# Performance work log

Measured on AMD Instinct MI355X. Metric: run time of the kernel, lower is better.

The kernel has to match this reference:

```python
import jax, jax.numpy as jnp
import numpy as np

B, H, T, TE = 48, 256, 512, 256  # batch*nodes, hidden=node_dim, timesteps, time_emb_dim


def timestep_embedding(ts, dim, max_positions=10000):
    half = dim // 2
    freqs = jnp.exp(jnp.arange(half, dtype=jnp.float32) * (-np.log(max_positions) / (half - 1)))
    e = ts.astype(jnp.float32)[:, None] * freqs[None, :]
    return jnp.concatenate([jnp.sin(e), jnp.cos(e)], axis=-1)  # [len, dim]


def mlp2(x, W1, b1, W2, b2):
    # 2-layer MLP: Linear -> SiLU -> Linear
    return jax.nn.silu(x @ W1 + b1) @ W2 + b2


def setup_inputs() -> dict:
    key = jax.random.key(0)
    ks = jax.random.split(key, 16)
    s = lambda k, shp, fan: (jax.random.normal(k, shp, dtype=jnp.float32) / np.sqrt(fan))
    return {
        "x": jax.random.normal(ks[0], (B, 3, T), dtype=jnp.float32),
        "h": jax.random.normal(ks[1], (B, H, T), dtype=jnp.float32),
        "qW1": s(ks[2], (H, H), H), "qb1": jnp.zeros((H,), jnp.float32),
        "qW2": s(ks[3], (H, H), H), "qb2": jnp.zeros((H,), jnp.float32),
        "kW1": s(ks[4], (H, H), H), "kb1": jnp.zeros((H,), jnp.float32),
        "kW2": s(ks[5], (H, H), H), "kb2": jnp.zeros((H,), jnp.float32),
        "vW1": s(ks[6], (H, H), H), "vb1": jnp.zeros((H,), jnp.float32),
        "vW2": s(ks[7], (H, H), H), "vb2": jnp.zeros((H,), jnp.float32),
        "xW1": s(ks[8], (H, H), H), "xb1": jnp.zeros((H,), jnp.float32),
        "xW2": s(ks[9], (H, 1), H), "xb2": jnp.zeros((1,), jnp.float32),
        "teW": s(ks[10], (TE, H), TE), "teb": jnp.zeros((H,), jnp.float32),
    }


def reference(x, h, qW1, qb1, qW2, qb2, kW1, kb1, kW2, kb2,
              vW1, vb1, vW2, vb2, xW1, xb1, xW2, xb2, teW, teb):
    Bb, _, Tt = x.shape
    rel_range = jnp.arange(-Tt + 1, Tt)
    emb_rel = timestep_embedding(rel_range, teW.shape[0]) @ teW + teb  # [2T-1, H]
    idx = jnp.arange(Tt)[:, None] - jnp.arange(Tt)[None, :] + (Tt - 1)  # [T, T]
    rel_pos = emb_rel[idx]  # [T, T, H]

    hm = h.transpose(0, 2, 1).reshape(Bb * Tt, -1)  # merge_time_dim: [BT, H]
    q = mlp2(hm, qW1, qb1, qW2, qb2)
    k = mlp2(hm, kW1, kb1, kW2, kb2)
    v = mlp2(hm, vW1, vb1, vW2, vb2)
    v_x = mlp2(v, xW1, xb1, xW2, xb2)  # [BT, 1]

    qt = q.reshape(Bb, Tt, -1)   # [B, T, H]
    kt = k.reshape(Bb, Tt, -1)
    vt = v.reshape(Bb, Tt, -1)

    base = jnp.einsum('bth,bsh->bts', qt, kt)  # [B, T, T]
    rel_logits = qt @ emb_rel.T  # [B, T, 2T-1]
    bias_logits = jnp.take_along_axis(
        rel_logits, jnp.broadcast_to(idx[None], (Bb, Tt, Tt)), axis=2)
    alpha = jax.nn.softmax(base + bias_logits, axis=-1)  # [B, T, T]

    std_vs = jnp.einsum('bts,bsh->bht', alpha, vt)       # [B, H, T]
    bias_h = jnp.einsum('bts,tsh->bht', alpha, rel_pos)  # [B, H, T]
    h_new = h + std_vs + bias_h

    # equivariant coord update: sum_s alpha[b,t,s]*(x[b,c,t]-x[b,c,s])*v_x[b,s]
    vx = v_x.reshape(Bb, Tt)               # [B, T]
    w = alpha * vx[:, None, :]             # [B, T, T]
    x_update = x * jnp.sum(w, axis=-1)[:, None, :] - jnp.einsum('bts,bcs->bct', w, x)
    x_new = x + x_update
    return (x_new, h_new)
```

## Files before the change

kernel.cpp:

```cpp
#include <hip/hip_runtime.h>
#include <math.h>

#define NB 48
#define HD 256
#define TS 512

typedef _Float16 f16x8 __attribute__((ext_vector_type(8)));
typedef float    f32x4 __attribute__((ext_vector_type(4)));

__device__ inline unsigned short f2h(float f) {
  union { _Float16 h; unsigned short u; } v; v.h = (_Float16)f; return v.u;
}
__device__ inline float h2f(unsigned short u) {
  union { unsigned short u; _Float16 h; } v; v.u = u; return (float)v.h;
}

#define ETS 1056

__device__ __forceinline__ void gll16(const void* g, void* l) {
  __builtin_amdgcn_global_load_lds(
      (const __attribute__((address_space(1))) unsigned int*)g,
      (__attribute__((address_space(3))) unsigned int*)l, 16, 0, 0);
}

__global__ __launch_bounds__(256) void k_prep(
    const float* __restrict__ h, unsigned short* __restrict__ hmH,
    float* __restrict__ vxZ,
    const float* __restrict__ w0, const float* __restrict__ w1,
    const float* __restrict__ w2, const float* __restrict__ w3,
    const float* __restrict__ w4, const float* __restrict__ w5,
    const float* __restrict__ w6, const float* __restrict__ w7,
    unsigned short* __restrict__ WtH, unsigned short* __restrict__ SC)
{
  const int gid = blockIdx.x;
  const int tid = threadIdx.x;

  if (gid < 128) {
    const int cf = tid & 127, half = tid >> 7;
    const float f = expf((float)cf * (-9.210340371976184f / 127.0f));
#pragma unroll
    for (int rr = 0; rr < 8; ++rr) {
      int r = gid * 8 + rr;
      float ang = (float)(r - (TS - 1)) * f;
      float val = (r == 1023) ? 0.0f : (half ? cosf(ang) : sinf(ang));
      SC[r * 256 + tid] = f2h(val);
    }
    return;
  }
  if (gid < 1664) {
    const int idx = gid - 128;
    const int bx = idx & 3, by = (idx >> 2) & 7, bz = idx >> 5;
    __shared__ float t[32 * 132];
    const int t0 = bx * 128, c0 = by * 32, b = bz;
    if (by == 0 && bz == 0) {
      float4* vz = (float4*)(vxZ + ((size_t)bx * 256 + tid) * 24);
#pragma unroll
      for (int i = 0; i < 6; ++i) vz[i] = make_float4(0.f, 0.f, 0.f, 0.f);
    }
#pragma unroll
    for (int i = 0; i < 4; ++i) {
      int cl = i * 8 + (tid >> 5);
      int t4 = (tid & 31) * 4;
      float4 v = *(const float4*)&h[((size_t)b * 256 + c0 + cl) * 512 + t0 + t4];
      t[cl * 132 + t4 + 0] = v.x; t[cl * 132 + t4 + 1] = v.y;
      t[cl * 132 + t4 + 2] = v.z; t[cl * 132 + t4 + 3] = v.w;
    }
    __syncthreads();
#pragma unroll
    for (int i = 0; i < 16; ++i) {
      int tl = i * 8 + (tid >> 5);
      int cl = tid & 31;
      hmH[((size_t)b * 512 + t0 + tl) * 256 + c0 + cl] = f2h(t[cl * 132 + tl]);
    }
    return;
  }
  {
    const int idx = gid - 1664;
    const int kx = idx & 3, ny = (idx >> 2) & 3, mat = idx >> 4;
    const float* W = (mat == 0) ? w0 : (mat == 1) ? w1 : (mat == 2) ? w2 :
                     (mat == 3) ? w3 : (mat == 4) ? w4 : (mat == 5) ? w5 :
                     (mat == 6) ? w6 : w7;
    unsigned short* dst = WtH + (size_t)mat * 65536;
    __shared__ float t[64 * 68];
    const int k0 = kx * 64, n0 = ny * 64;
#pragma unroll
    for (int i = 0; i < 4; ++i) {
      int kr = i * 16 + (tid >> 4);
      int nc = (tid & 15) * 4;
      float4 v = *(const float4*)&W[(size_t)(k0 + kr) * 256 + n0 + nc];
      t[kr * 68 + nc + 0] = v.x; t[kr * 68 + nc + 1] = v.y;
      t[kr * 68 + nc + 2] = v.z; t[kr * 68 + nc + 3] = v.w;
    }
    __syncthreads();
#pragma unroll
    for (int i = 0; i < 4; ++i) {
      int nr = i * 16 + (tid >> 4);
      int kc = (tid & 15) * 4;
#pragma unroll
      for (int j = 0; j < 4; ++j)
        dst[(size_t)(n0 + nr) * 256 + k0 + kc + j] = f2h(t[(kc + j) * 68 + nr]);
    }
  }
}

struct MJob {
  const unsigned short* A; const unsigned short* W1; const float* b1;
  const unsigned short* W2; const float* b2;
  unsigned short* outB; unsigned short* outT;
};
struct MJobs { MJob j[3]; };

__global__ __launch_bounds__(256) void k_mlp2(MJobs jobs)
{
  __shared__ __align__(16) char Wst[32768];
  __shared__ __align__(16) char Ast[8192];
  __shared__ __align__(16) char Hst[64 * 528];

  const MJob jb = jobs.j[blockIdx.y];
  const int tid  = threadIdx.x;
  const int lane = tid & 63;
  const int w    = tid >> 6;
  const int rq   = lane & 15;
  const int kq   = lane >> 4;
  const int m0   = blockIdx.x * 64;
  const char* Ag  = (const char*)jb.A  + (size_t)m0 * 512;
  const char* W1g = (const char*)jb.W1;
  const char* W2g = (const char*)jb.W2;

  f32x4 acc[4][4];
#pragma unroll
  for (int mi = 0; mi < 4; ++mi)
#pragma unroll
    for (int ni = 0; ni < 4; ++ni) acc[mi][ni] = (f32x4){0.f, 0.f, 0.f, 0.f};

  for (int kt = 0; kt < 4; ++kt) {
    __syncthreads();
#pragma unroll
    for (int i = 0; i < 2; ++i) {
      int c = i * 256 + tid;
      int row = c >> 3, ch = c & 7;
      int colg = (ch * 16) ^ ((row & 7) << 4);
      gll16(Ag + (size_t)row * 512 + kt * 128 + colg, Ast + i * 4096 + w * 1024);
    }
#pragma unroll
    for (int i = 0; i < 8; ++i) {
      int c = i * 256 + tid;
      int row = c >> 3, ch = c & 7;
      int colg = (ch * 16) ^ ((row & 7) << 4);
      gll16(W1g + (size_t)row * 512 + kt * 128 + colg, Wst + i * 4096 + w * 1024);
    }
    __syncthreads();
#pragma unroll
    for (int ks = 0; ks < 2; ++ks) {
      const int kb = ks * 64 + kq * 16;
      f16x8 af[4], bfr[4];
#pragma unroll
      for (int mi = 0; mi < 4; ++mi) {
        int row = mi * 16 + rq;
        af[mi] = *(const f16x8*)(Ast + row * 128 + (kb ^ ((row & 7) << 4)));
      }
#pragma unroll
      for (int ni = 0; ni < 4; ++ni) {
        int row = w * 64 + ni * 16 + rq;
        bfr[ni] = *(const f16x8*)(Wst + row * 128 + (kb ^ ((row & 7) << 4)));
      }
#pragma unroll
      for (int mi = 0; mi < 4; ++mi)
#pragma unroll
        for (int ni = 0; ni < 4; ++ni)
          acc[mi][ni] = __builtin_amdgcn_mfma_f32_16x16x32_f16(
              af[mi], bfr[ni], acc[mi][ni], 0, 0, 0);
    }
  }
  {
#pragma unroll
    for (int ni = 0; ni < 4; ++ni) {
      const int n = w * 64 + ni * 16 + rq;
      const float bv = jb.b1[n];
#pragma unroll
      for (int mi = 0; mi < 4; ++mi)
#pragma unroll
        for (int j = 0; j < 4; ++j) {
          float vl = acc[mi][ni][j] + bv;
          vl = vl / (1.0f + __expf(-vl));
          int m = mi * 16 + kq * 4 + j;
          *(unsigned short*)(Hst + m * 528 + n * 2) = f2h(vl);
        }
    }
  }
#pragma unroll
  for (int mi = 0; mi < 4; ++mi)
#pragma unroll
    for (int ni = 0; ni < 4; ++ni) acc[mi][ni] = (f32x4){0.f, 0.f, 0.f, 0.f};

  for (int kt = 0; kt < 4; ++kt) {
    __syncthreads();
#pragma unroll
    for (int i = 0; i < 8; ++i) {
      int c = i * 256 + tid;
      int row = c >> 3, ch = c & 7;
      int colg = (ch * 16) ^ ((row & 7) << 4);
      gll16(W2g + (size_t)row * 512 + kt * 128 + colg, Wst + i * 4096 + w * 1024);
    }
    __syncthreads();
#pragma unroll
    for (int ks = 0; ks < 2; ++ks) {
      const int kb = ks * 64 + kq * 16;
      f16x8 af[4], bfr[4];
#pragma unroll
      for (int mi = 0; mi < 4; ++mi) {
        int row = mi * 16 + rq;
        af[mi] = *(const f16x8*)(Hst + row * 528 + kt * 128 + kb);
      }
#pragma unroll
      for (int ni = 0; ni < 4; ++ni) {
        int row = w * 64 + ni * 16 + rq;
        bfr[ni] = *(const f16x8*)(Wst + row * 128 + (kb ^ ((row & 7) << 4)));
      }
#pragma unroll
      for (int mi = 0; mi < 4; ++mi)
#pragma unroll
        for (int ni = 0; ni < 4; ++ni)
          acc[mi][ni] = __builtin_amdgcn_mfma_f32_16x16x32_f16(
              af[mi], bfr[ni], acc[mi][ni], 0, 0, 0);
    }
  }

  const int bb = m0 >> 9;
  const int tbase = m0 & 511;
#pragma unroll
  for (int ni = 0; ni < 4; ++ni) {
    const int n = w * 64 + ni * 16 + rq;
    const float bv = jb.b2[n];
#pragma unroll
    for (int mi = 0; mi < 4; ++mi) {
      float vl4[4];
#pragma unroll
      for (int j = 0; j < 4; ++j) vl4[j] = acc[mi][ni][j] + bv;
#pragma unroll
      for (int j = 0; j < 4; ++j) {
        int m = m0 + mi * 16 + kq * 4 + j;
        jb.outB[(size_t)m * 256 + n] = f2h(vl4[j]);
      }
      if (jb.outT) {
        ushort4 o;
        o.x = f2h(vl4[0]); o.y = f2h(vl4[1]);
        o.z = f2h(vl4[2]); o.w = f2h(vl4[3]);
        *(ushort4*)&jb.outT[((size_t)(bb * 256 + n) << 9) +
                            tbase + mi * 16 + kq * 4] = o;
      }
    }
  }
}

struct GJob {
  const unsigned short* A; const unsigned short* Wt; const float* bias;
  unsigned short* outB; unsigned short* outE;
  const float* vxW; float* vxOut;
  int act; int mMax;
};
struct GJobs { GJob j[2]; };

__global__ __launch_bounds__(512) void k_gemm(GJobs jobs)
{
  __shared__ __align__(16) char AsB[16384];
  __shared__ __align__(16) char WsB[32768];

  const GJob jb = jobs.j[blockIdx.z];
  const int m0 = blockIdx.x * 128;
  if (m0 >= jb.mMax) return;

  const int tid  = threadIdx.x;
  const int lane = tid & 63;
  const int w    = tid >> 6;
  const int wr   = w >> 2, wc = w & 3;
  const int rq   = lane & 15;
  const int kq   = lane >> 4;

  const char* Ag = (const char*)jb.A + (size_t)m0 * 512;
  const char* Wg = (const char*)jb.Wt;

  f32x4 acc[4][4];
#pragma unroll
  for (int mi = 0; mi < 4; ++mi)
#pragma unroll
    for (int ni = 0; ni < 4; ++ni) acc[mi][ni] = (f32x4){0.f, 0.f, 0.f, 0.f};

  for (int kt = 0; kt < 4; ++kt) {
    __syncthreads();
#pragma unroll
    for (int i = 0; i < 2; ++i) {
      int c = i * 512 + tid;
      int row = c >> 3, ch = c & 7;
      int colg = (ch * 16) ^ ((row & 7) << 4);
      gll16(Ag + (size_t)row * 512 + kt * 128 + colg, AsB + i * 8192 + w * 1024);
    }
#pragma unroll
    for (int i = 0; i < 4; ++i) {
      int c = i * 512 + tid;
      int row = c >> 3, ch = c & 7;
      int colg = (ch * 16) ^ ((row & 7) << 4);
      gll16(Wg + (size_t)row * 512 + kt * 128 + colg, WsB + i * 8192 + w * 1024);
    }
    __syncthreads();
#pragma unroll
    for (int ks = 0; ks < 2; ++ks) {
      const int kb = ks * 64 + kq * 16;
      f16x8 af[4], bfr[4];
#pragma unroll
      for (int mi = 0; mi < 4; ++mi) {
        int row = wr * 64 + mi * 16 + rq;
        af[mi] = *(const f16x8*)(AsB + row * 128 + (kb ^ ((row & 7) << 4)));
      }
#pragma unroll
      for (int ni = 0; ni < 4; ++ni) {
        int row = wc * 64 + ni * 16 + rq;
        bfr[ni] = *(const f16x8*)(WsB + row * 128 + (kb ^ ((row & 7) << 4)));
      }
#pragma unroll
      for (int mi = 0; mi < 4; ++mi)
#pragma unroll
        for (int ni = 0; ni < 4; ++ni)
          acc[mi][ni] = __builtin_amdgcn_mfma_f32_16x16x32_f16(
              af[mi], bfr[ni], acc[mi][ni], 0, 0, 0);
    }
  }

  float bv[4];
#pragma unroll
  for (int ni = 0; ni < 4; ++ni)
    bv[ni] = jb.bias[wc * 64 + ni * 16 + rq];

  float vxp_[4][4];
#pragma unroll
  for (int mi = 0; mi < 4; ++mi)
#pragma unroll
    for (int j = 0; j < 4; ++j) vxp_[mi][j] = 0.f;

#pragma unroll
  for (int mi = 0; mi < 4; ++mi) {
#pragma unroll
    for (int ni = 0; ni < 4; ++ni) {
      const int n = wc * 64 + ni * 16 + rq;
      float vl4[4];
#pragma unroll
      for (int j = 0; j < 4; ++j) {
        float vl = acc[mi][ni][j] + bv[ni];
        if (jb.act) vl = vl / (1.0f + __expf(-vl));
        vl4[j] = vl;
      }
      const int mb = m0 + wr * 64 + mi * 16 + kq * 4;
      if (jb.outB) {
#pragma unroll
        for (int j = 0; j < 4; ++j)
          jb.outB[(size_t)(mb + j) * 256 + n] = f2h(vl4[j]);
      }
      if (jb.outE) {
#pragma unroll
        for (int j = 0; j < 4; ++j)
          jb.outE[(size_t)n * ETS + mb + j] = f2h(vl4[j]);
      }
      if (jb.vxOut) {
        float wq = jb.vxW[n];
#pragma unroll
        for (int j = 0; j < 4; ++j) vxp_[mi][j] = fmaf(vl4[j], wq, vxp_[mi][j]);
      }
    }
  }

  if (jb.vxOut) {
#pragma unroll
    for (int mi = 0; mi < 4; ++mi)
#pragma unroll
      for (int j = 0; j < 4; ++j) {
        float s = vxp_[mi][j];
        s += __shfl_xor(s, 1); s += __shfl_xor(s, 2);
        s += __shfl_xor(s, 4); s += __shfl_xor(s, 8);
        if (rq == 0)
          atomicAdd(&jb.vxOut[m0 + wr * 64 + mi * 16 + kq * 4 + j], s);
      }
  }
}

__global__ __launch_bounds__(256, 2) void k_attn6(
    const float* __restrict__ xin, const float* __restrict__ hin,
    const unsigned short* __restrict__ qH, const unsigned short* __restrict__ kH,
    const unsigned short* __restrict__ vtH, const float* __restrict__ vxm,
    const float* __restrict__ xb2p,
    const unsigned short* __restrict__ embB, const unsigned short* __restrict__ embT,
    float* __restrict__ xout, float* __restrict__ hout)
{
  __shared__ __align__(16) char smem[70656];
  float* S  = (float*)smem;
  unsigned short* Pb = (unsigned short*)smem;
  unsigned short* Pe = (unsigned short*)(smem + 33280);

  const int tid  = threadIdx.x;
  const int lane = tid & 63;
  const int w    = tid >> 6;
  const int rq   = lane & 15;
  const int kq   = lane >> 4;
  const int id = blockIdx.x;
  const int t0 = ((id >> 3) & 15) * 32;
  const int b  = (id & 7) + 8 * (id >> 7);
  const int sw = w * 128;

  f16x8 q0[8], q1[8];
  {
    const size_t qo = ((size_t)(b * TS + t0 + rq) << 8) + kq * 8;
#pragma unroll
    for (int ks = 0; ks < 8; ++ks) {
      q0[ks] = *(const f16x8*)(qH + qo + ks * 32);
      q1[ks] = *(const f16x8*)(qH + qo + 4096 + ks * 32);
    }
  }

  f32x4 a0[8], a1[8];
#pragma unroll
  for (int ni = 0; ni < 8; ++ni) {
    a0[ni] = (f32x4){0.f, 0.f, 0.f, 0.f};
    a1[ni] = (f32x4){0.f, 0.f, 0.f, 0.f};
  }
  {
    const unsigned short* kp = kH + ((size_t)(b * TS + sw + rq) << 8) + kq * 8;
    f16x8 kA[8], kB[8];
#pragma unroll
    for (int ni = 0; ni < 8; ++ni) kA[ni] = *(const f16x8*)(kp + ni * 4096);
#pragma unroll
    for (int ni = 0; ni < 8; ++ni) kB[ni] = *(const f16x8*)(kp + ni * 4096 + 32);
#pragma unroll
    for (int ks = 0; ks < 8; ks += 2) {
#pragma unroll
      for (int ni = 0; ni < 8; ++ni) {
        a0[ni] = __builtin_amdgcn_mfma_f32_16x16x32_f16(q0[ks], kA[ni], a0[ni], 0, 0, 0);
        a1[ni] = __builtin_amdgcn_mfma_f32_16x16x32_f16(q1[ks], kA[ni], a1[ni], 0, 0, 0);
        if (ks + 2 < 8) kA[ni] = *(const f16x8*)(kp + ni * 4096 + (ks + 2) * 32);
      }
#pragma unroll
      for (int ni = 0; ni < 8; ++ni) {
        a0[ni] = __builtin_amdgcn_mfma_f32_16x16x32_f16(q0[ks + 1], kB[ni], a0[ni], 0, 0, 0);
        a1[ni] = __builtin_amdgcn_mfma_f32_16x16x32_f16(q1[ks + 1], kB[ni], a1[ni], 0, 0, 0);
        if (ks + 3 < 8) kB[ni] = *(const f16x8*)(kp + ni * 4096 + (ks + 3) * 32);
      }
    }
  }

  const int rbR = t0 - sw + 384;
  const unsigned short* ep = embB + ((size_t)(rbR + rq) << 8) + kq * 8;
  f16x8 eA[10], eB[10];
#pragma unroll
  for (int f = 0; f < 10; ++f) eA[f] = *(const f16x8*)(ep + f * 4096);
#pragma unroll
  for (int ni = 0; ni < 8; ++ni)
#pragma unroll
    for (int j = 0; j < 4; ++j) {
      S[(kq * 4 + j) * 524 + sw + ni * 16 + rq]        = a0[ni][j];
      S[(16 + kq * 4 + j) * 524 + sw + ni * 16 + rq]   = a1[ni][j];
    }
#pragma unroll
  for (int f = 0; f < 10; ++f) eB[f] = *(const f16x8*)(ep + f * 4096 + 32);

  f32x4 r0[9], r1[9];
#pragma unroll
  for (int ni = 0; ni < 9; ++ni) {
    r0[ni] = (f32x4){0.f, 0.f, 0.f, 0.f};
    r1[ni] = (f32x4){0.f, 0.f, 0.f, 0.f};
  }
#pragma unroll
  for (int ks = 0; ks < 8; ks += 2) {
#pragma unroll
    for (int f = 0; f < 10; ++f) {
      if (f < 9) r0[f] = __builtin_amdgcn_mfma_f32_16x16x32_f16(q0[ks], eA[f], r0[f], 0, 0, 0);
      if (f > 0) r1[f - 1] = __builtin_amdgcn_mfma_f32_16x16x32_f16(q1[ks], eA[f], r1[f - 1], 0, 0, 0);
      if (ks + 2 < 8) eA[f] = *(const f16x8*)(ep + f * 4096 + (ks + 2) * 32);
    }
#pragma unroll
    for (int f = 0; f < 10; ++f) {
      if (f < 9) r0[f] = __builtin_amdgcn_mfma_f32_16x16x32_f16(q0[ks + 1], eB[f], r0[f], 0, 0, 0);
      if (f > 0) r1[f - 1] = __builtin_amdgcn_mfma_f32_16x16x32_f16(q1[ks + 1], eB[f], r1[f - 1], 0, 0, 0);
      if (ks + 3 < 8) eB[f] = *(const f16x8*)(ep + f * 4096 + (ks + 3) * 32);
    }
  }

  asm volatile("s_waitcnt lgkmcnt(0)" ::: "memory");
  __builtin_amdgcn_sched_barrier(0);
#pragma unroll
  for (int ni = 0; ni < 9; ++ni)
#pragma unroll
    for (int j = 0; j < 4; ++j) {
      int tp  = kq * 4 + j;
      int slw = tp + 127 - (ni * 16 + rq);
      if (slw >= 0 && slw < 128) {
        S[tp * 524 + sw + slw]        += r0[ni][j];
        S[(16 + tp) * 524 + sw + slw] += r1[ni][j];
      }
    }
  __syncthreads();

  const int row16 = tid >> 4, tx = tid & 15;
  float p0[32], p1[32];
  float invl0, invl1;
#pragma unroll
  for (int pass = 0; pass < 2; ++pass) {
    float* pp = pass ? p1 : p0;
    const float* Srow = S + (pass * 16 + row16) * 524 + tx * 4;
    float mx = -3.0e38f, l = 0.f;
#pragma unroll
    for (int i = 0; i < 8; ++i) {
      float4 v = *(const float4*)(Srow + i * 64);
      pp[4*i+0] = v.x; pp[4*i+1] = v.y; pp[4*i+2] = v.z; pp[4*i+3] = v.w;
    }
#pragma unroll
    for (int i = 0; i < 32; ++i) mx = fmaxf(mx, pp[i]);
    mx = fmaxf(mx, __shfl_xor(mx, 1)); mx = fmaxf(mx, __shfl_xor(mx, 2));
    mx = fmaxf(mx, __shfl_xor(mx, 4)); mx = fmaxf(mx, __shfl_xor(mx, 8));
#pragma unroll
    for (int i = 0; i < 32; ++i) { pp[i] = __expf(pp[i] - mx); l += pp[i]; }
    l += __shfl_xor(l, 1); l += __shfl_xor(l, 2);
    l += __shfl_xor(l, 4); l += __shfl_xor(l, 8);
    if (pass) invl1 = 1.0f / l; else invl0 = 1.0f / l;
  }

  {
    const float xb2c = xb2p[0];
    const float* vxp = vxm + b * TS;
    const float* xp  = xin + (size_t)b * 3 * TS;
    float w0s = 0.f, xa00 = 0.f, xa01 = 0.f, xa02 = 0.f;
    float w1s = 0.f, xa10 = 0.f, xa11 = 0.f, xa12 = 0.f;
#pragma unroll
    for (int i = 0; i < 8; ++i) {
      int s = i * 64 + tx * 4;
      float4 vv = *(const float4*)(vxp + s);
      float4 x0 = *(const float4*)(xp + s);
      float4 x1 = *(const float4*)(xp + TS + s);
      float4 x2 = *(const float4*)(xp + 2 * TS + s);
      float vb0 = vv.x + xb2c, vb1 = vv.y + xb2c, vb2 = vv.z + xb2c, vb3 = vv.w + xb2c;
      float wv;
      wv = p0[4*i+0] * vb0; w0s += wv; xa00 = fmaf(wv, x0.x, xa00); xa01 = fmaf(wv, x1.x, xa01); xa02 = fmaf(wv, x2.x, xa02);
      wv = p0[4*i+1] * vb1; w0s += wv; xa00 = fmaf(wv, x0.y, xa00); xa01 = fmaf(wv, x1.y, xa01); xa02 = fmaf(wv, x2.y, xa02);
      wv = p0[4*i+2] * vb2; w0s += wv; xa00 = fmaf(wv, x0.z, xa00); xa01 = fmaf(wv, x1.z, xa01); xa02 = fmaf(wv, x2.z, xa02);
      wv = p0[4*i+3] * vb3; w0s += wv; xa00 = fmaf(wv, x0.w, xa00); xa01 = fmaf(wv, x1.w, xa01); xa02 = fmaf(wv, x2.w, xa02);
      wv = p1[4*i+0] * vb0; w1s += wv; xa10 = fmaf(wv, x0.x, xa10); xa11 = fmaf(wv, x1.x, xa11); xa12 = fmaf(wv, x2.x, xa12);
      wv = p1[4*i+1] * vb1; w1s += wv; xa10 = fmaf(wv, x0.y, xa10); xa11 = fmaf(wv, x1.y, xa11); xa12 = fmaf(wv, x2.y, xa12);
      wv = p1[4*i+2] * vb2; w1s += wv; xa10 = fmaf(wv, x0.z, xa10); xa11 = fmaf(wv, x1.z, xa11); xa12 = fmaf(wv, x2.z, xa12);
      wv = p1[4*i+3] * vb3; w1s += wv; xa10 = fmaf(wv, x0.w, xa10); xa11 = fmaf(wv, x1.w, xa11); xa12 = fmaf(wv, x2.w, xa12);
    }
#pragma unroll
    for (int m = 1; m < 16; m <<= 1) {
      w0s += __shfl_xor(w0s, m); xa00 += __shfl_xor(xa00, m);
      xa01 += __shfl_xor(xa01, m); xa02 += __shfl_xor(xa02, m);
      w1s += __shfl_xor(w1s, m); xa10 += __shfl_xor(xa10, m);
      xa11 += __shfl_xor(xa11, m); xa12 += __shfl_xor(xa12, m);
    }
    if (tx == 0) {
      int ta = t0 + row16, tb2 = t0 + 16 + row16;
      float wsa = w0s * invl0, wsb = w1s * invl1;
      xout[(b * 3 + 0) * TS + ta] = xp[ta]          * (1.0f + wsa) - xa00 * invl0;
      xout[(b * 3 + 1) * TS + ta] = xp[TS + ta]     * (1.0f + wsa) - xa01 * invl0;
      xout[(b * 3 + 2) * TS + ta] = xp[2 * TS + ta] * (1.0f + wsa) - xa02 * invl0;
      xout[(b * 3 + 0) * TS + tb2] = xp[tb2]          * (1.0f + wsb) - xa10 * invl1;
      xout[(b * 3 + 1) * TS + tb2] = xp[TS + tb2]     * (1.0f + wsb) - xa11 * invl1;
      xout[(b * 3 + 2) * TS + tb2] = xp[2 * TS + tb2] * (1.0f + wsb) - xa12 * invl1;
    }
  }
  __syncthreads();

  {
    unsigned int* pz = (unsigned int*)Pe;
    for (int i = tid; i < 9344; i += 256) pz[i] = 0u;
  }
  __syncthreads();

#pragma unroll
  for (int pass = 0; pass < 2; ++pass) {
    const float* pp = pass ? p1 : p0;
    const float il = pass ? invl1 : invl0;
    const int row = pass * 16 + row16;
    unsigned short* pbrow = Pb + row * 520 + tx * 4;
    unsigned short* perow = Pe + row * 584 + row + 511;
#pragma unroll
    for (int i = 0; i < 8; ++i) {
      int s = i * 64 + tx * 4;
      ushort4 pu;
      pu.x = f2h(pp[4*i+0] * il); pu.y = f2h(pp[4*i+1] * il);
      pu.z = f2h(pp[4*i+2] * il); pu.w = f2h(pp[4*i+3] * il);
      *(ushort4*)(pbrow + i * 64) = pu;
      perow[-(s + 0)] = pu.x; perow[-(s + 1)] = pu.y;
      perow[-(s + 2)] = pu.z; perow[-(s + 3)] = pu.w;
    }
  }
  __syncthreads();

  const int n0 = w * 64;
  f32x4 o0[4], o1[4];
#pragma unroll
  for (int ni = 0; ni < 4; ++ni) {
    o0[ni] = (f32x4){0.f, 0.f, 0.f, 0.f};
    o1[ni] = (f32x4){0.f, 0.f, 0.f, 0.f};
  }
  {
    const unsigned short* pb0 = Pb + rq * 520 + kq * 8;
    const unsigned short* pb1 = Pb + (16 + rq) * 520 + kq * 8;
    const unsigned short* pe0 = Pe + rq * 584 + kq * 8;
    const unsigned short* pe1 = Pe + (16 + rq) * 584 + kq * 8;
    const unsigned short* vtp = vtH + ((size_t)(b * 256 + n0 + rq) << 9) + kq * 8;
    const unsigned short* etp = embT + (size_t)(n0 + rq) * ETS + t0 + kq * 8;
    f16x8 vA[4], vB[4], gA[4], gB[4];
#pragma unroll
    for (int ni = 0; ni < 4; ++ni) {
      vA[ni] = *(const f16x8*)(vtp + ni * 8192);
      gA[ni] = *(const f16x8*)(etp + ni * 16 * ETS);
      vB[ni] = *(const f16x8*)(vtp + ni * 8192 + 32);
      gB[ni] = *(const f16x8*)(etp + ni * 16 * ETS + 32);
    }
#pragma unroll
    for (int kk = 0; kk < 16; kk += 2) {
      f16x8 pa0 = *(const f16x8*)(pb0 + kk * 32);
      f16x8 pa1 = *(const f16x8*)(pb1 + kk * 32);
#pragma unroll
      for (int ni = 0; ni < 4; ++ni) {
        o0[ni] = __builtin_amdgcn_mfma_f32_16x16x32_f16(pa0, vA[ni], o0[ni], 0, 0, 0);
        o1[ni] = __builtin_amdgcn_mfma_f32_16x16x32_f16(pa1, vA[ni], o1[ni], 0, 0, 0);
        if (kk + 2 < 16) vA[ni] = *(const f16x8*)(vtp + ni * 8192 + (kk + 2) * 32);
      }
      f16x8 pe0f = *(const f16x8*)(pe0 + kk * 32);
      f16x8 pe1f = *(const f16x8*)(pe1 + kk * 32);
#pragma unroll
      for (int ni = 0; ni < 4; ++ni) {
        o0[ni] = __builtin_amdgcn_mfma_f32_16x16x32_f16(pe0f, gA[ni], o0[ni], 0, 0, 0);
        o1[ni] = __builtin_amdgcn_mfma_f32_16x16x32_f16(pe1f, gA[ni], o1[ni], 0, 0, 0);
        if (kk + 2 < 17) gA[ni] = *(const f16x8*)(etp + ni * 16 * ETS + (kk + 2) * 32);
      }
      f16x8 pc0 = *(const f16x8*)(pb0 + (kk + 1) * 32);
      f16x8 pc1 = *(const f16x8*)(pb1 + (kk + 1) * 32);
#pragma unroll
      for (int ni = 0; ni < 4; ++ni) {
        o0[ni] = __builtin_amdgcn_mfma_f32_16x16x32_f16(pc0, vB[ni], o0[ni], 0, 0, 0);
        o1[ni] = __builtin_amdgcn_mfma_f32_16x16x32_f16(pc1, vB[ni], o1[ni], 0, 0, 0);
        if (kk + 3 < 16) vB[ni] = *(const f16x8*)(vtp + ni * 8192 + (kk + 3) * 32);
      }
      f16x8 pd0 = *(const f16x8*)(pe0 + (kk + 1) * 32);
      f16x8 pd1 = *(const f16x8*)(pe1 + (kk + 1) * 32);
#pragma unroll
      for (int ni = 0; ni < 4; ++ni) {
        o0[ni] = __builtin_amdgcn_mfma_f32_16x16x32_f16(pd0, gB[ni], o0[ni], 0, 0, 0);
        o1[ni] = __builtin_amdgcn_mfma_f32_16x16x32_f16(pd1, gB[ni], o1[ni], 0, 0, 0);
        if (kk + 3 < 17) gB[ni] = *(const f16x8*)(etp + ni * 16 * ETS + (kk + 3) * 32);
      }
    }
    f16x8 pt0 = *(const f16x8*)(pe0 + 16 * 32);
    f16x8 pt1 = *(const f16x8*)(pe1 + 16 * 32);
#pragma unroll
    for (int ni = 0; ni < 4; ++ni) {
      o0[ni] = __builtin_amdgcn_mfma_f32_16x16x32_f16(pt0, gA[ni], o0[ni], 0, 0, 0);
      o1[ni] = __builtin_amdgcn_mfma_f32_16x16x32_f16(pt1, gA[ni], o1[ni], 0, 0, 0);
    }
  }

  {
#pragma unroll
    for (int ni = 0; ni < 4; ++ni) {
      int hh = n0 + ni * 16 + rq;
      size_t base = (((size_t)(b * 256 + hh)) << 9) + t0 + kq * 4;
      float4 hv0 = *(const float4*)(hin + base);
      float4 ov0;
      ov0.x = hv0.x + o0[ni][0];
      ov0.y = hv0.y + o0[ni][1];
      ov0.z = hv0.z + o0[ni][2];
      ov0.w = hv0.w + o0[ni][3];
      *(float4*)(hout + base) = ov0;
      float4 hv1 = *(const float4*)(hin + base + 16);
      float4 ov1;
      ov1.x = hv1.x + o1[ni][0];
      ov1.y = hv1.y + o1[ni][1];
      ov1.z = hv1.z + o1[ni][2];
      ov1.w = hv1.w + o1[ni][3];
      *(float4*)(hout + base + 16) = ov1;
    }
  }
}

extern "C" void kernel_launch(void* const* d_in, const int* in_sizes, int n_in,
                              void* d_out, int out_size, void* d_ws, size_t ws_size,
                              hipStream_t stream)
{
  const float* x   = (const float*)d_in[0];
  const float* h   = (const float*)d_in[1];
  const float* qW1 = (const float*)d_in[2];
  const float* qb1 = (const float*)d_in[3];
  const float* qW2 = (const float*)d_in[4];
  const float* qb2 = (const float*)d_in[5];
  const float* kW1 = (const float*)d_in[6];
  const float* kb1 = (const float*)d_in[7];
  const float* kW2 = (const float*)d_in[8];
  const float* kb2 = (const float*)d_in[9];
  const float* vW1 = (const float*)d_in[10];
  const float* vb1 = (const float*)d_in[11];
  const float* vW2 = (const float*)d_in[12];
  const float* vb2 = (const float*)d_in[13];
  const float* xW1 = (const float*)d_in[14];
  const float* xb1 = (const float*)d_in[15];
  const float* xW2 = (const float*)d_in[16];
  const float* xb2 = (const float*)d_in[17];
  const float* teW = (const float*)d_in[18];
  const float* teb = (const float*)d_in[19];

  unsigned short* cur = (unsigned short*)d_ws;
  unsigned short* embB = cur; cur += 1024 * 256;
  unsigned short* embT = cur; cur += 256 * ETS;
  unsigned short* SC   = cur; cur += 1024 * 256;
  unsigned short* hmH  = cur; cur += (size_t)24576 * 256;
  unsigned short* WtH  = cur; cur += 8 * 65536;
  unsigned short* qHp  = cur; cur += (size_t)24576 * 256;
  unsigned short* kHp  = cur; cur += (size_t)24576 * 256;
  unsigned short* vHp  = cur; cur += (size_t)24576 * 256;
  unsigned short* vtH  = cur; cur += (size_t)24576 * 256;
  float* vx = (float*)cur;

  float* xout = (float*)d_out;
  float* hout = xout + NB * 3 * TS;

  k_prep<<<1792, 256, 0, stream>>>(h, hmH, vx,
                                   qW1, qW2, kW1, kW2, vW1, vW2, xW1, teW,
                                   WtH, SC);

  {
    MJobs jm{{{hmH, WtH + 0 * 65536, qb1, WtH + 1 * 65536, qb2, qHp, nullptr},
              {hmH, WtH + 2 * 65536, kb1, WtH + 3 * 65536, kb2, kHp, nullptr},
              {hmH, WtH + 4 * 65536, vb1, WtH + 5 * 65536, vb2, vHp, vtH}}};
    k_mlp2<<<dim3(384, 3), 256, 0, stream>>>(jm);
  }

  {
    GJobs jg{{{SC,  WtH + 7 * 65536, teb, embB, embT, nullptr, nullptr, 0, 1024},
              {vHp, WtH + 6 * 65536, xb1, nullptr, nullptr, xW2, vx, 1, 24576}}};
    k_gemm<<<dim3(192, 1, 2), 512, 0, stream>>>(jg);
  }

  k_attn6<<<768, 256, 0, stream>>>(x, h, qHp, kHp, vtH, vx, xb2,
                                   embB, embT, xout, hout);
}
```

Before: 190.2 us.

## Fuse x-MLP first layer and time-embedding GEMM into the MLP kernel

Extends the MLP kernel with an optional third GEMM stage: the v-path now applies xW1, SiLU and the xW2 dot product in place, reducing to the vx output with atomics. This drops the separate general GEMM kernel and the round trip of the full v activation through global memory. The time-embedding projection becomes a fourth job of the same launch that skips the second layer and writes both layouts. The cost is that v-path blocks now run three chained GEMMs, so work per block is uneven across the grid.

```diff
diff --git a/kernel.cpp b/kernel.cpp
--- a/kernel.cpp
+++ b/kernel.cpp
@@ -106,9 +106,12 @@
 struct MJob {
   const unsigned short* A; const unsigned short* W1; const float* b1;
   const unsigned short* W2; const float* b2;
-  unsigned short* outB; unsigned short* outT;
+  unsigned short* outB; unsigned short* outT; unsigned short* outE;
+  const unsigned short* W3; const float* b3;
+  const float* vxW; float* vxOut;
+  int mMax;
 };
-struct MJobs { MJob j[3]; };
+struct MJobs { MJob j[4]; };
 
 __global__ __launch_bounds__(256) void k_mlp2(MJobs jobs)
 {
@@ -117,15 +120,16 @@
   __shared__ __align__(16) char Hst[64 * 528];
 
   const MJob jb = jobs.j[blockIdx.y];
+  const int m0 = blockIdx.x * 64;
+  if (m0 >= jb.mMax) return;
+
   const int tid  = threadIdx.x;
   const int lane = tid & 63;
   const int w    = tid >> 6;
   const int rq   = lane & 15;
   const int kq   = lane >> 4;
-  const int m0   = blockIdx.x * 64;
-  const char* Ag  = (const char*)jb.A  + (size_t)m0 * 512;
+  const char* Ag  = (const char*)jb.A + (size_t)m0 * 512;
   const char* W1g = (const char*)jb.W1;
-  const char* W2g = (const char*)jb.W2;
 
   f32x4 acc[4][4];
 #pragma unroll
@@ -172,6 +176,25 @@
               af[mi], bfr[ni], acc[mi][ni], 0, 0, 0);
     }
   }
+
+  if (!jb.W2) {
+#pragma unroll
+    for (int ni = 0; ni < 4; ++ni) {
+      const int n = w * 64 + ni * 16 + rq;
+      const float bv = jb.b1[n];
+#pragma unroll
+      for (int mi = 0; mi < 4; ++mi)
+#pragma unroll
+        for (int j = 0; j < 4; ++j) {
+          float vl = acc[mi][ni][j] + bv;
+          int m = m0 + mi * 16 + kq * 4 + j;
+          jb.outB[(size_t)m * 256 + n] = f2h(vl);
+          jb.outE[(size_t)n * ETS + m] = f2h(vl);
+        }
+    }
+    return;
+  }
+
   {
 #pragma unroll
     for (int ni = 0; ni < 4; ++ni) {
@@ -193,6 +216,7 @@
 #pragma unroll
     for (int ni = 0; ni < 4; ++ni) acc[mi][ni] = (f32x4){0.f, 0.f, 0.f, 0.f};
 
+  const char* W2g = (const char*)jb.W2;
   for (int kt = 0; kt < 4; ++kt) {
     __syncthreads();
 #pragma unroll
@@ -237,10 +261,12 @@
       float vl4[4];
 #pragma unroll
       for (int j = 0; j < 4; ++j) vl4[j] = acc[mi][ni][j] + bv;
-#pragma unroll
-      for (int j = 0; j < 4; ++j) {
-        int m = m0 + mi * 16 + kq * 4 + j;
-        jb.outB[(size_t)m * 256 + n] = f2h(vl4[j]);
+      if (jb.outB) {
+#pragma unroll
+        for (int j = 0; j < 4; ++j) {
+          int m = m0 + mi * 16 + kq * 4 + j;
+          jb.outB[(size_t)m * 256 + n] = f2h(vl4[j]);
+        }
       }
       if (jb.outT) {
         ushort4 o;
@@ -251,56 +277,38 @@
       }
     }
   }
-}
-
-struct GJob {
-  const unsigned short* A; const unsigned short* Wt; const float* bias;
-  unsigned short* outB; unsigned short* outE;
-  const float* vxW; float* vxOut;
-  int act; int mMax;
-};
-struct GJobs { GJob j[2]; };
-
-__global__ __launch_bounds__(512) void k_gemm(GJobs jobs)
-{
-  __shared__ __align__(16) char AsB[16384];
-  __shared__ __align__(16) char WsB[32768];
-
-  const GJob jb = jobs.j[blockIdx.z];
-  const int m0 = blockIdx.x * 128;
-  if (m0 >= jb.mMax) return;
-
-  const int tid  = threadIdx.x;
-  const int lane = tid & 63;
-  const int w    = tid >> 6;
-  const int wr   = w >> 2, wc = w & 3;
-  const int rq   = lane & 15;
-  const int kq   = lane >> 4;
-
-  const char* Ag = (const char*)jb.A + (size_t)m0 * 512;
-  const char* Wg = (const char*)jb.Wt;
-
-  f32x4 acc[4][4];
+
+  if (!jb.W3) return;
+
+  __syncthreads();
+  {
+#pragma unroll
+    for (int ni = 0; ni < 4; ++ni) {
+      const int n = w * 64 + ni * 16 + rq;
+      const float bv = jb.b2[n];
+#pragma unroll
+      for (int mi = 0; mi < 4; ++mi)
+#pragma unroll
+        for (int j = 0; j < 4; ++j) {
+          int m = mi * 16 + kq * 4 + j;
+          *(unsigned short*)(Hst + m * 528 + n * 2) = f2h(acc[mi][ni][j] + bv);
+        }
+    }
+  }
 #pragma unroll
   for (int mi = 0; mi < 4; ++mi)
 #pragma unroll
     for (int ni = 0; ni < 4; ++ni) acc[mi][ni] = (f32x4){0.f, 0.f, 0.f, 0.f};
 
+  const char* W3g = (const char*)jb.W3;
   for (int kt = 0; kt < 4; ++kt) {
     __syncthreads();
 #pragma unroll
-    for (int i = 0; i < 2; ++i) {
-      int c = i * 512 + tid;
+    for (int i = 0; i < 8; ++i) {
+      int c = i * 256 + tid;
       int row = c >> 3, ch = c & 7;
       int colg = (ch * 16) ^ ((row & 7) << 4);
-      gll16(Ag + (size_t)row * 512 + kt * 128 + colg, AsB + i * 8192 + w * 1024);
-    }
-#pragma unroll
-    for (int i = 0; i < 4; ++i) {
-      int c = i * 512 + tid;
-      int row = c >> 3, ch = c & 7;
-      int colg = (ch * 16) ^ ((row & 7) << 4);
-      gll16(Wg + (size_t)row * 512 + kt * 128 + colg, WsB + i * 8192 + w * 1024);
+      gll16(W3g + (size_t)row * 512 + kt * 128 + colg, Wst + i * 4096 + w * 1024);
     }
     __syncthreads();
 #pragma unroll
@@ -309,13 +317,13 @@
       f16x8 af[4], bfr[4];
 #pragma unroll
       for (int mi = 0; mi < 4; ++mi) {
-        int row = wr * 64 + mi * 16 + rq;
-        af[mi] = *(const f16x8*)(AsB + row * 128 + (kb ^ ((row & 7) << 4)));
+        int row = mi * 16 + rq;
+        af[mi] = *(const f16x8*)(Hst + row * 528 + kt * 128 + kb);
       }
 #pragma unroll
       for (int ni = 0; ni < 4; ++ni) {
-        int row = wc * 64 + ni * 16 + rq;
-        bfr[ni] = *(const f16x8*)(WsB + row * 128 + (kb ^ ((row & 7) << 4)));
+        int row = w * 64 + ni * 16 + rq;
+        bfr[ni] = *(const f16x8*)(Wst + row * 128 + (kb ^ ((row & 7) << 4)));
       }
 #pragma unroll
       for (int mi = 0; mi < 4; ++mi)
@@ -326,49 +334,26 @@
     }
   }
 
-  float bv[4];
-#pragma unroll
-  for (int ni = 0; ni < 4; ++ni)
-    bv[ni] = jb.bias[wc * 64 + ni * 16 + rq];
-
-  float vxp_[4][4];
-#pragma unroll
-  for (int mi = 0; mi < 4; ++mi)
-#pragma unroll
-    for (int j = 0; j < 4; ++j) vxp_[mi][j] = 0.f;
-
-#pragma unroll
-  for (int mi = 0; mi < 4; ++mi) {
+  {
+    float vxp_[4][4];
+#pragma unroll
+    for (int mi = 0; mi < 4; ++mi)
+#pragma unroll
+      for (int j = 0; j < 4; ++j) vxp_[mi][j] = 0.f;
 #pragma unroll
     for (int ni = 0; ni < 4; ++ni) {
-      const int n = wc * 64 + ni * 16 + rq;
-      float vl4[4];
-#pragma unroll
-      for (int j = 0; j < 4; ++j) {
-        float vl = acc[mi][ni][j] + bv[ni];
-        if (jb.act) vl = vl / (1.0f + __expf(-vl));
-        vl4[j] = vl;
-      }
-      const int mb = m0 + wr * 64 + mi * 16 + kq * 4;
-      if (jb.outB) {
-#pragma unroll
-        for (int j = 0; j < 4; ++j)
-          jb.outB[(size_t)(mb + j) * 256 + n] = f2h(vl4[j]);
-      }
-      if (jb.outE) {
-#pragma unroll
-        for (int j = 0; j < 4; ++j)
-          jb.outE[(size_t)n * ETS + mb + j] = f2h(vl4[j]);
-      }
-      if (jb.vxOut) {
-        float wq = jb.vxW[n];
-#pragma unroll
-        for (int j = 0; j < 4; ++j) vxp_[mi][j] = fmaf(vl4[j], wq, vxp_[mi][j]);
-      }
-    }
-  }
-
-  if (jb.vxOut) {
+      const int n = w * 64 + ni * 16 + rq;
+      const float bv = jb.b3[n];
+      const float wq = jb.vxW[n];
+#pragma unroll
+      for (int mi = 0; mi < 4; ++mi)
+#pragma unroll
+        for (int j = 0; j < 4; ++j) {
+          float vl = acc[mi][ni][j] + bv;
+          vl = vl / (1.0f + __expf(-vl));
+          vxp_[mi][j] = fmaf(vl, wq, vxp_[mi][j]);
+        }
+    }
 #pragma unroll
     for (int mi = 0; mi < 4; ++mi)
 #pragma unroll
@@ -377,7 +362,7 @@
         s += __shfl_xor(s, 1); s += __shfl_xor(s, 2);
         s += __shfl_xor(s, 4); s += __shfl_xor(s, 8);
         if (rq == 0)
-          atomicAdd(&jb.vxOut[m0 + wr * 64 + mi * 16 + kq * 4 + j], s);
+          atomicAdd(&jb.vxOut[m0 + mi * 16 + kq * 4 + j], s);
       }
   }
 }
@@ -713,7 +698,6 @@
   unsigned short* WtH  = cur; cur += 8 * 65536;
   unsigned short* qHp  = cur; cur += (size_t)24576 * 256;
   unsigned short* kHp  = cur; cur += (size_t)24576 * 256;
-  unsigned short* vHp  = cur; cur += (size_t)24576 * 256;
   unsigned short* vtH  = cur; cur += (size_t)24576 * 256;
   float* vx = (float*)cur;
 
@@ -725,16 +709,17 @@
                                    WtH, SC);
 
   {
-    MJobs jm{{{hmH, WtH + 0 * 65536, qb1, WtH + 1 * 65536, qb2, qHp, nullptr},
-              {hmH, WtH + 2 * 65536, kb1, WtH + 3 * 65536, kb2, kHp, nullptr},
-              {hmH, WtH + 4 * 65536, vb1, WtH + 5 * 65536, vb2, vHp, vtH}}};
-    k_mlp2<<<dim3(384, 3), 256, 0, stream>>>(jm);
-  }
-
-  {
-    GJobs jg{{{SC,  WtH + 7 * 65536, teb, embB, embT, nullptr, nullptr, 0, 1024},
-              {vHp, WtH + 6 * 65536, xb1, nullptr, nullptr, xW2, vx, 1, 24576}}};
-    k_gemm<<<dim3(192, 1, 2), 512, 0, stream>>>(jg);
+    MJobs jm{{
+      {hmH, WtH + 0 * 65536, qb1, WtH + 1 * 65536, qb2,
+       qHp, nullptr, nullptr, nullptr, nullptr, nullptr, nullptr, 24576},
+      {hmH, WtH + 2 * 65536, kb1, WtH + 3 * 65536, kb2,
+       kHp, nullptr, nullptr, nullptr, nullptr, nullptr, nullptr, 24576},
+      {hmH, WtH + 4 * 65536, vb1, WtH + 5 * 65536, vb2,
+       nullptr, vtH, nullptr, WtH + 6 * 65536, xb1, xW2, vx, 24576},
+      {SC,  WtH + 7 * 65536, teb, nullptr, nullptr,
+       embB, nullptr, embT, nullptr, nullptr, nullptr, nullptr, 1024}
+    }};
+    k_mlp2<<<dim3(384, 4), 256, 0, stream>>>(jm);
   }
 
   k_attn6<<<768, 256, 0, stream>>>(x, h, qHp, kHp, vtH, vx, xb2,
```

After: 203.4 us. +6.9%, slower.
